# Optimization experiments

Hardware: AMD Instinct MI355X
Metric: run time of the kernel (lower is better)

## Reference

```python
import jax, jax.numpy as jnp
import numpy as np

B, S, N = 8, 64, 256
STATE, IN_F, OUT_F = 128, 64, 64
ALPHA = 0.2
NEG = -9e15


def setup_inputs() -> dict:
    key = jax.random.key(0)
    ks = jax.random.split(key, 12)
    d = {
        "hyper_inputs": jax.random.normal(ks[0], (B, S, STATE), jnp.float32),
        "inputs": jax.random.normal(ks[1], (B, S, N, IN_F), jnp.float32),
        "Adj": jax.random.randint(ks[2], (N, N), 0, 2, jnp.int32),
        # hyper_w: Linear(STATE,32) -> ReLU -> Linear(32, OUT_F*IN_F)
        "w1": jax.random.normal(ks[3], (STATE, 32), jnp.float32) * 0.08,
        "b1": jax.random.normal(ks[4], (32,), jnp.float32) * 0.01,
        "w2": jax.random.normal(ks[5], (32, OUT_F * IN_F), jnp.float32) * 0.08,
        "b2": jax.random.normal(ks[6], (OUT_F * IN_F,), jnp.float32) * 0.01,
        # hyper_a: Linear(STATE,32) -> ReLU -> Linear(32, 2*OUT_F)
        "aw1": jax.random.normal(ks[7], (STATE, 32), jnp.float32) * 0.08,
        "ab1": jax.random.normal(ks[8], (32,), jnp.float32) * 0.01,
        "aw2": jax.random.normal(ks[9], (32, 2 * OUT_F), jnp.float32) * 0.08,
        "ab2": jax.random.normal(ks[10], (2 * OUT_F,), jnp.float32) * 0.01,
    }
    return d


def _leaky(x):
    return jnp.where(x >= 0, x, ALPHA * x)


def reference(hyper_inputs, inputs, Adj, w1, b1, w2, b2, aw1, ab1, aw2, ab2):
    # hypernetwork-generated per-(b,s) weights
    hdn = jax.nn.relu(hyper_inputs @ w1 + b1)            # [B,S,32]
    W = jnp.abs(hdn @ w2 + b2).reshape(B, S, IN_F, OUT_F)
    hda = jax.nn.relu(hyper_inputs @ aw1 + ab1)
    a = jnp.abs(hda @ aw2 + ab2)                          # [B,S,2*OUT_F]

    h = jnp.einsum('bsni,bsio->bsno', inputs, W)          # [B,S,N,OUT_F]

    # decomposed GAT scores: e[b,s,i,j] = leakyrelu(h_i.a1 + h_j.a2)
    a1, a2 = a[..., :OUT_F], a[..., OUT_F:]
    e1 = jnp.einsum('bsno,bso->bsn', h, a1)               # source term
    e2 = jnp.einsum('bsno,bso->bsn', h, a2)               # target term
    e = _leaky(e1[..., :, None] + e2[..., None, :])       # [B,S,N,N]

    attention = jnp.where(Adj > 0, e, NEG)
    # NOTE: faithful to original: softmax over dim=1 (the S axis)
    attention = jax.nn.softmax(attention, axis=1)
    h_prime = jnp.einsum('bsij,bsjo->bsio', attention, h)  # [B,S,N,OUT_F]
    return jax.nn.elu(h_prime)                              # concat=True branch
```

## Files before the change

kernel.cpp:

```cpp
#include <hip/hip_runtime.h>
#include <hip/hip_bf16.h>
#include <math.h>

#define BB 8
#define SS 64
#define NN 256
#define ST 128
#define IF 64
#define OF 64
#define H1 32
#define ALPHA 0.2f

typedef short short8 __attribute__((ext_vector_type(8)));
typedef float f32x4 __attribute__((ext_vector_type(4)));
typedef unsigned short ushort_t;

static __device__ __forceinline__ ushort_t f2bf(float f) {
    __hip_bfloat16 h = __float2bfloat16(f);
    return *reinterpret_cast<ushort_t*>(&h);
}

__global__ __launch_bounds__(512) void k_hyper2(
    const float* __restrict__ hyper,
    const float* __restrict__ w1, const float* __restrict__ b1,
    const float* __restrict__ w2, const float* __restrict__ b2,
    const float* __restrict__ aw1, const float* __restrict__ ab1,
    const float* __restrict__ aw2, const float* __restrict__ ab2,
    float* __restrict__ Wd, float* __restrict__ Aa)
{
    const int t = threadIdx.x;
    const int bs0 = blockIdx.x * 2;
    __shared__ float hy[2][ST];
    __shared__ float hdn_s[2][H1];
    __shared__ float hda_s[2][H1];
    if (t < 2 * ST)
        hy[t >> 7][t & 127] = hyper[(size_t)bs0 * ST + t];
    __syncthreads();
    if (t < 64) {
        const int q = t >> 5, c = t & 31;
        float acc = b1[c];
#pragma unroll 4
        for (int k = 0; k < ST; ++k) acc = fmaf(hy[q][k], w1[k * H1 + c], acc);
        hdn_s[q][c] = fmaxf(acc, 0.f);
    } else if (t < 128) {
        const int tt = t - 64;
        const int q = tt >> 5, c = tt & 31;
        float acc = ab1[c];
#pragma unroll 4
        for (int k = 0; k < ST; ++k) acc = fmaf(hy[q][k], aw1[k * H1 + c], acc);
        hda_s[q][c] = fmaxf(acc, 0.f);
    }
    __syncthreads();
    if (t < 256) {
        const int q = t >> 7, c = t & 127;
        float a = ab2[c];
#pragma unroll
        for (int k = 0; k < H1; ++k)
            a = fmaf(hda_s[q][k], aw2[k * 128 + c], a);
        Aa[(size_t)(bs0 + q) * 128 + c] = fabsf(a);
    }
#pragma unroll
    for (int p = 0; p < 2; ++p) {
        const int e = t * 4 + p * 2048;
        const float4 bb = *(const float4*)&b2[e];
        float4 a0 = bb, a1 = bb;
#pragma unroll
        for (int kq = 0; kq < 8; ++kq) {
            const float4 h0 = *(const float4*)&hdn_s[0][kq * 4];
            const float4 h1 = *(const float4*)&hdn_s[1][kq * 4];
#pragma unroll
            for (int c = 0; c < 4; ++c) {
                const float4 wv = *(const float4*)&w2[(size_t)(kq * 4 + c) * 4096 + e];
                const float s0 = (c == 0) ? h0.x : (c == 1) ? h0.y : (c == 2) ? h0.z : h0.w;
                const float s1 = (c == 0) ? h1.x : (c == 1) ? h1.y : (c == 2) ? h1.z : h1.w;
                a0.x = fmaf(s0, wv.x, a0.x); a0.y = fmaf(s0, wv.y, a0.y);
                a0.z = fmaf(s0, wv.z, a0.z); a0.w = fmaf(s0, wv.w, a0.w);
                a1.x = fmaf(s1, wv.x, a1.x); a1.y = fmaf(s1, wv.y, a1.y);
                a1.z = fmaf(s1, wv.z, a1.z); a1.w = fmaf(s1, wv.w, a1.w);
            }
        }
        a0.x = fabsf(a0.x); a0.y = fabsf(a0.y); a0.z = fabsf(a0.z); a0.w = fabsf(a0.w);
        a1.x = fabsf(a1.x); a1.y = fabsf(a1.y); a1.z = fabsf(a1.z); a1.w = fabsf(a1.w);
        *(float4*)&Wd[(size_t)(bs0 + 0) * 4096 + e] = a0;
        *(float4*)&Wd[(size_t)(bs0 + 1) * 4096 + e] = a1;
    }
}

__global__ __launch_bounds__(256) void k_h(
    const float* __restrict__ x, const float* __restrict__ Wd,
    const float* __restrict__ Aa,
    ushort_t* __restrict__ HbT, float* __restrict__ E1, float* __restrict__ E2)
{
    const int bs = blockIdx.x;
    const int tid = threadIdx.x;
    const int nt = tid >> 3;
    const int ot = tid & 7;
    __shared__ float Wl[IF * OF];
    __shared__ float a1s[OF], a2s[OF];
    {
        const float4* src = (const float4*)(Wd + (size_t)bs * 4096);
        float4* dst = (float4*)Wl;
        for (int p = 0; p < 4; ++p) dst[tid + p * 256] = src[tid + p * 256];
        if (tid < 64) a1s[tid] = Aa[(size_t)bs * 128 + tid];
        else if (tid < 128) a2s[tid - 64] = Aa[(size_t)bs * 128 + tid];
    }
    __syncthreads();

    const float4* xb = (const float4*)(x + ((size_t)bs * NN + nt * 8) * IF);
    float acc[8][8];
#pragma unroll
    for (int r = 0; r < 8; ++r)
#pragma unroll
        for (int c = 0; c < 8; ++c) acc[r][c] = 0.f;

#pragma unroll
    for (int kq = 0; kq < 16; ++kq) {
        float4 xv[8];
#pragma unroll
        for (int r = 0; r < 8; ++r) xv[r] = xb[r * 16 + kq];
#pragma unroll
        for (int c = 0; c < 4; ++c) {
            const int k = kq * 4 + c;
            const float4 w0 = *(const float4*)&Wl[k * OF + ot * 8];
            const float4 w1 = *(const float4*)&Wl[k * OF + ot * 8 + 4];
#pragma unroll
            for (int r = 0; r < 8; ++r) {
                const float xs = (c == 0) ? xv[r].x : (c == 1) ? xv[r].y
                               : (c == 2) ? xv[r].z : xv[r].w;
                acc[r][0] = fmaf(xs, w0.x, acc[r][0]);
                acc[r][1] = fmaf(xs, w0.y, acc[r][1]);
                acc[r][2] = fmaf(xs, w0.z, acc[r][2]);
                acc[r][3] = fmaf(xs, w0.w, acc[r][3]);
                acc[r][4] = fmaf(xs, w1.x, acc[r][4]);
                acc[r][5] = fmaf(xs, w1.y, acc[r][5]);
                acc[r][6] = fmaf(xs, w1.z, acc[r][6]);
                acc[r][7] = fmaf(xs, w1.w, acc[r][7]);
            }
        }
    }

    const float4 av0 = *(const float4*)&a1s[ot * 8];
    const float4 av1 = *(const float4*)&a1s[ot * 8 + 4];
    const float4 bv0 = *(const float4*)&a2s[ot * 8];
    const float4 bv1 = *(const float4*)&a2s[ot * 8 + 4];
    float e1sel = 0.f, e2sel = 0.f;
#pragma unroll
    for (int r = 0; r < 8; ++r) {
        float p1 = acc[r][0]*av0.x + acc[r][1]*av0.y + acc[r][2]*av0.z + acc[r][3]*av0.w
                 + acc[r][4]*av1.x + acc[r][5]*av1.y + acc[r][6]*av1.z + acc[r][7]*av1.w;
        float p2 = acc[r][0]*bv0.x + acc[r][1]*bv0.y + acc[r][2]*bv0.z + acc[r][3]*bv0.w
                 + acc[r][4]*bv1.x + acc[r][5]*bv1.y + acc[r][6]*bv1.z + acc[r][7]*bv1.w;
        p1 += __shfl_xor(p1, 1, 64); p2 += __shfl_xor(p2, 1, 64);
        p1 += __shfl_xor(p1, 2, 64); p2 += __shfl_xor(p2, 2, 64);
        p1 += __shfl_xor(p1, 4, 64); p2 += __shfl_xor(p2, 4, 64);
        if (ot == r) { e1sel = p1; e2sel = p2; }
    }
    E1[(size_t)bs * NN + tid] = e1sel;
    E2[(size_t)bs * NN + tid] = e2sel;

    ushort_t* hb = HbT + (size_t)bs * (OF * NN);
#pragma unroll
    for (int c = 0; c < 8; ++c) {
        short8 pk;
#pragma unroll
        for (int r = 0; r < 8; ++r) pk[r] = (short)f2bf(acc[r][c]);
        *(short8*)(hb + (size_t)(ot * 8 + c) * NN + nt * 8) = pk;
    }
}

__global__ __launch_bounds__(256) void k_softstats(
    const float* __restrict__ E1, const float* __restrict__ E2,
    const int* __restrict__ Adj, unsigned int* __restrict__ MR)
{
    const int bid = blockIdx.x;
    const int b = bid >> 6, i0 = (bid & 63) * 4;
    const int t = threadIdx.x;
    __shared__ float e1s[4][SS];
    {
        const int ii = t >> 6, s = t & 63;
        e1s[ii][s] = E1[(size_t)(b * SS + s) * NN + i0 + ii];
    }
    float e2r[SS];
#pragma unroll
    for (int s = 0; s < SS; ++s)
        e2r[s] = E2[(size_t)(b * SS + s) * NN + t];
    __syncthreads();

#pragma unroll
    for (int ii = 0; ii < 4; ++ii) {
        float mx = -3.0e38f;
#pragma unroll
        for (int s = 0; s < SS; ++s) {
            float v = e1s[ii][s] + e2r[s];
            v = (v >= 0.f) ? v : ALPHA * v;
            mx = fmaxf(mx, v);
        }
        const unsigned int mu = (unsigned int)f2bf(mx);
        const float mUse = __uint_as_float(mu << 16);
        float sum = 0.f;
#pragma unroll
        for (int s = 0; s < SS; ++s) {
            float v = e1s[ii][s] + e2r[s];
            v = (v >= 0.f) ? v : ALPHA * v;
            sum += __expf(v - mUse);
        }
        const int adj = Adj[(size_t)(i0 + ii) * NN + t];
        const float r = (adj > 0) ? (1.f / sum) : -0.015625f;
        MR[(size_t)(b * NN + i0 + ii) * NN + t] =
            (mu << 16) | (unsigned int)f2bf(r);
    }
}

__global__ __launch_bounds__(512) void k_attn(
    const ushort_t* __restrict__ HbT, const float* __restrict__ E1,
    const float* __restrict__ E2, const unsigned int* __restrict__ MR,
    float* __restrict__ out)
{
    const int bs = blockIdx.x;
    const int b = bs >> 6;
    const int tid = threadIdx.x;
    const int wid = tid >> 6;
    const int lane = tid & 63;
    const int l15 = lane & 15;
    const int lhi = lane >> 4;

    __shared__ float e2s[NN];
    if (tid < NN) e2s[tid] = E2[(size_t)bs * NN + tid];
    __syncthreads();

    float e1r[2];
#pragma unroll
    for (int mt = 0; mt < 2; ++mt)
        e1r[mt] = E1[(size_t)bs * NN + wid * 32 + mt * 16 + l15];

    f32x4 acc[2][4];
#pragma unroll
    for (int mt = 0; mt < 2; ++mt)
#pragma unroll
        for (int nt = 0; nt < 4; ++nt) acc[mt][nt] = (f32x4){0.f, 0.f, 0.f, 0.f};

    const ushort_t* hb = HbT + (size_t)bs * (OF * NN);
    const unsigned int* mrb = MR + ((size_t)b * NN) * NN;

    for (int ch = 0; ch < 4; ++ch) {
        short8 bf[4][2];
#pragma unroll
        for (int nt = 0; nt < 4; ++nt) {
            const int o = nt * 16 + l15;
#pragma unroll
            for (int ks = 0; ks < 2; ++ks) {
                const int j0 = ch * 64 + ks * 32 + lhi * 8;
                bf[nt][ks] = *(const short8*)(hb + (size_t)o * NN + j0);
            }
        }
        float e2v[2][8];
#pragma unroll
        for (int ks = 0; ks < 2; ++ks) {
            const int k0 = ch * 64 + ks * 32 + lhi * 8;
            const float4 lo = *(const float4*)&e2s[k0];
            const float4 hi = *(const float4*)&e2s[k0 + 4];
            e2v[ks][0] = lo.x; e2v[ks][1] = lo.y; e2v[ks][2] = lo.z; e2v[ks][3] = lo.w;
            e2v[ks][4] = hi.x; e2v[ks][5] = hi.y; e2v[ks][6] = hi.z; e2v[ks][7] = hi.w;
        }
#pragma unroll
        for (int mt = 0; mt < 2; ++mt) {
            const int row = wid * 32 + mt * 16 + l15;
            const float e1v = e1r[mt];
            const uint4* mrow = (const uint4*)(mrb + (size_t)row * NN);
            short8 af[2];
#pragma unroll
            for (int ks = 0; ks < 2; ++ks) {
                const int k0 = ch * 64 + ks * 32 + lhi * 8;
                const uint4 m0 = mrow[k0 >> 2];
                const uint4 m1 = mrow[(k0 >> 2) + 1];
                const unsigned int wv[8] = {m0.x, m0.y, m0.z, m0.w,
                                            m1.x, m1.y, m1.z, m1.w};
                short8 pk;
#pragma unroll
                for (int kk = 0; kk < 8; ++kk) {
                    const float Mf = __uint_as_float(wv[kk] & 0xFFFF0000u);
                    const float Rf = __uint_as_float(wv[kk] << 16);
                    float v = e1v + e2v[ks][kk];
                    v = (v >= 0.f) ? v : ALPHA * v;
                    const float a = (Rf < 0.f) ? -Rf : __expf(v - Mf) * Rf;
                    pk[kk] = (short)f2bf(a);
                }
                af[ks] = pk;
            }
#pragma unroll
            for (int nt = 0; nt < 4; ++nt) {
                acc[mt][nt] = __builtin_amdgcn_mfma_f32_16x16x32_bf16(
                    af[0], bf[nt][0], acc[mt][nt], 0, 0, 0);
                acc[mt][nt] = __builtin_amdgcn_mfma_f32_16x16x32_bf16(
                    af[1], bf[nt][1], acc[mt][nt], 0, 0, 0);
            }
        }
    }

    float* ob = out + (size_t)bs * (NN * OF);
#pragma unroll
    for (int mt = 0; mt < 2; ++mt) {
        const int rbase = wid * 32 + mt * 16 + lhi * 4;
#pragma unroll
        for (int nt = 0; nt < 4; ++nt) {
            const int o = nt * 16 + l15;
#pragma unroll
            for (int reg = 0; reg < 4; ++reg) {
                float v = acc[mt][nt][reg];
                v = (v > 0.f) ? v : (__expf(v) - 1.f);
                ob[(size_t)(rbase + reg) * OF + o] = v;
            }
        }
    }
}

extern "C" void kernel_launch(void* const* d_in, const int* in_sizes, int n_in,
                              void* d_out, int out_size, void* d_ws, size_t ws_size,
                              hipStream_t stream)
{
    const float* hyper = (const float*)d_in[0];
    const float* x     = (const float*)d_in[1];
    const int*   Adj   = (const int*)d_in[2];
    const float* w1    = (const float*)d_in[3];
    const float* b1    = (const float*)d_in[4];
    const float* w2    = (const float*)d_in[5];
    const float* b2    = (const float*)d_in[6];
    const float* aw1   = (const float*)d_in[7];
    const float* ab1   = (const float*)d_in[8];
    const float* aw2   = (const float*)d_in[9];
    const float* ab2   = (const float*)d_in[10];
    float* out = (float*)d_out;

    float* ws      = (float*)d_ws;
    float* Wd      = ws;
    float* Aa      = Wd + 2097152;
    ushort_t* HbT  = (ushort_t*)(Aa + 65536);
    float* E1      = (float*)(HbT + 8388608);
    float* E2      = E1 + 131072;
    unsigned int* MRp = (unsigned int*)(E2 + 131072);

    k_hyper2<<<dim3(256), dim3(512), 0, stream>>>(hyper, w1, b1, w2, b2,
                                                  aw1, ab1, aw2, ab2, Wd, Aa);
    k_h<<<dim3(512), dim3(256), 0, stream>>>(x, Wd, Aa, HbT, E1, E2);
    k_softstats<<<dim3(512), dim3(256), 0, stream>>>(E1, E2, Adj, MRp);
    k_attn<<<dim3(512), dim3(512), 0, stream>>>(HbT, E1, E2, MRp, out);
}
```

Before: 90.75 us.

## Use bf16 MFMA for projection, fold attention vectors, switch to exp2 math

The per-(b,s) projection h = x·W moves from scalar FP32 FMAs to bf16 MFMA. W is staged transposed in LDS with an XOR swizzle to avoid bank conflicts. E1/E2 are now computed as x·(W·a), pre-scaled by log2(e), so exp2f can replace __expf in the softstats and attention kernels. The softstats kernel caches leaky values in registers instead of recomputing them, and the attention kernel hoists its MR loads ahead of the compute loop. The change trades FP32 precision in h for bf16 inputs to the MFMA.

```diff
diff --git a/kernel.cpp b/kernel.cpp
--- a/kernel.cpp
+++ b/kernel.cpp
@@ -10,8 +10,10 @@
 #define OF 64
 #define H1 32
 #define ALPHA 0.2f
+#define LOG2E 1.4426950408889634f
 
 typedef short short8 __attribute__((ext_vector_type(8)));
+typedef short short4_t __attribute__((ext_vector_type(4)));
 typedef float f32x4 __attribute__((ext_vector_type(4)));
 typedef unsigned short ushort_t;
 
@@ -93,78 +95,122 @@
 {
     const int bs = blockIdx.x;
     const int tid = threadIdx.x;
-    const int nt = tid >> 3;
-    const int ot = tid & 7;
-    __shared__ float Wl[IF * OF];
+    const int wid = tid >> 6;
+    const int lane = tid & 63;
+    const int l15 = lane & 15;
+    const int lhi = lane >> 4;
+
+    __shared__ ushort_t Wt[IF * OF];
+    __shared__ float wa1s[IF], wa2s[IF];
     __shared__ float a1s[OF], a2s[OF];
+
+    if (tid < 64) a1s[tid] = Aa[(size_t)bs * 128 + tid];
+    else if (tid < 128) a2s[tid - 64] = Aa[(size_t)bs * 128 + tid];
+
     {
-        const float4* src = (const float4*)(Wd + (size_t)bs * 4096);
-        float4* dst = (float4*)Wl;
-        for (int p = 0; p < 4; ++p) dst[tid + p * 256] = src[tid + p * 256];
-        if (tid < 64) a1s[tid] = Aa[(size_t)bs * 128 + tid];
-        else if (tid < 128) a2s[tid - 64] = Aa[(size_t)bs * 128 + tid];
-    }
-    __syncthreads();
-
-    const float4* xb = (const float4*)(x + ((size_t)bs * NN + nt * 8) * IF);
-    float acc[8][8];
-#pragma unroll
-    for (int r = 0; r < 8; ++r)
-#pragma unroll
-        for (int c = 0; c < 8; ++c) acc[r][c] = 0.f;
-
-#pragma unroll
-    for (int kq = 0; kq < 16; ++kq) {
-        float4 xv[8];
-#pragma unroll
-        for (int r = 0; r < 8; ++r) xv[r] = xb[r * 16 + kq];
-#pragma unroll
-        for (int c = 0; c < 4; ++c) {
-            const int k = kq * 4 + c;
-            const float4 w0 = *(const float4*)&Wl[k * OF + ot * 8];
-            const float4 w1 = *(const float4*)&Wl[k * OF + ot * 8 + 4];
-#pragma unroll
-            for (int r = 0; r < 8; ++r) {
-                const float xs = (c == 0) ? xv[r].x : (c == 1) ? xv[r].y
-                               : (c == 2) ? xv[r].z : xv[r].w;
-                acc[r][0] = fmaf(xs, w0.x, acc[r][0]);
-                acc[r][1] = fmaf(xs, w0.y, acc[r][1]);
-                acc[r][2] = fmaf(xs, w0.z, acc[r][2]);
-                acc[r][3] = fmaf(xs, w0.w, acc[r][3]);
-                acc[r][4] = fmaf(xs, w1.x, acc[r][4]);
-                acc[r][5] = fmaf(xs, w1.y, acc[r][5]);
-                acc[r][6] = fmaf(xs, w1.z, acc[r][6]);
-                acc[r][7] = fmaf(xs, w1.w, acc[r][7]);
-            }
-        }
-    }
-
-    const float4 av0 = *(const float4*)&a1s[ot * 8];
-    const float4 av1 = *(const float4*)&a1s[ot * 8 + 4];
-    const float4 bv0 = *(const float4*)&a2s[ot * 8];
-    const float4 bv1 = *(const float4*)&a2s[ot * 8 + 4];
-    float e1sel = 0.f, e2sel = 0.f;
-#pragma unroll
-    for (int r = 0; r < 8; ++r) {
-        float p1 = acc[r][0]*av0.x + acc[r][1]*av0.y + acc[r][2]*av0.z + acc[r][3]*av0.w
-                 + acc[r][4]*av1.x + acc[r][5]*av1.y + acc[r][6]*av1.z + acc[r][7]*av1.w;
-        float p2 = acc[r][0]*bv0.x + acc[r][1]*bv0.y + acc[r][2]*bv0.z + acc[r][3]*bv0.w
-                 + acc[r][4]*bv1.x + acc[r][5]*bv1.y + acc[r][6]*bv1.z + acc[r][7]*bv1.w;
-        p1 += __shfl_xor(p1, 1, 64); p2 += __shfl_xor(p2, 1, 64);
-        p1 += __shfl_xor(p1, 2, 64); p2 += __shfl_xor(p2, 2, 64);
-        p1 += __shfl_xor(p1, 4, 64); p2 += __shfl_xor(p2, 4, 64);
-        if (ot == r) { e1sel = p1; e2sel = p2; }
-    }
-    E1[(size_t)bs * NN + tid] = e1sel;
-    E2[(size_t)bs * NN + tid] = e2sel;
+        const float4* w4 = (const float4*)(Wd + (size_t)bs * 4096);
+#pragma unroll
+        for (int p = 0; p < 4; ++p) {
+            const int idx = tid + p * 256;
+            const float4 f = w4[idx];
+            const int k = (idx * 4) >> 6;
+            const int o0 = (idx * 4) & 63;
+            Wt[(o0 + 0) * 64 + (k ^ (((o0 + 0) & 7) << 3))] = f2bf(f.x);
+            Wt[(o0 + 1) * 64 + (k ^ (((o0 + 1) & 7) << 3))] = f2bf(f.y);
+            Wt[(o0 + 2) * 64 + (k ^ (((o0 + 2) & 7) << 3))] = f2bf(f.z);
+            Wt[(o0 + 3) * 64 + (k ^ (((o0 + 3) & 7) << 3))] = f2bf(f.w);
+        }
+    }
+    __syncthreads();
+
+    if (tid < 64) {
+        const float4* wr = (const float4*)(Wd + (size_t)bs * 4096 + tid * 64);
+        float s1 = 0.f, s2 = 0.f;
+#pragma unroll
+        for (int q = 0; q < 16; ++q) {
+            const float4 f = wr[q];
+            const float4 u = *(const float4*)&a1s[q * 4];
+            const float4 v = *(const float4*)&a2s[q * 4];
+            s1 += f.x * u.x + f.y * u.y + f.z * u.z + f.w * u.w;
+            s2 += f.x * v.x + f.y * v.y + f.z * v.z + f.w * v.w;
+        }
+        wa1s[tid] = s1; wa2s[tid] = s2;
+    }
+    __syncthreads();
+
+    {
+        const float4* xr = (const float4*)(x + ((size_t)bs * NN + tid) * IF);
+        float s1 = 0.f, s2 = 0.f;
+#pragma unroll
+        for (int q = 0; q < 16; ++q) {
+            const float4 f = xr[q];
+            const float4 u = *(const float4*)&wa1s[q * 4];
+            const float4 v = *(const float4*)&wa2s[q * 4];
+            s1 += f.x * u.x + f.y * u.y + f.z * u.z + f.w * u.w;
+            s2 += f.x * v.x + f.y * v.y + f.z * v.z + f.w * v.w;
+        }
+        E1[(size_t)bs * NN + tid] = s1 * LOG2E;
+        E2[(size_t)bs * NN + tid] = s2 * LOG2E;
+    }
+
+    f32x4 acc[4][4];
+#pragma unroll
+    for (int mt = 0; mt < 4; ++mt)
+#pragma unroll
+        for (int nt = 0; nt < 4; ++nt) acc[mt][nt] = (f32x4){0.f, 0.f, 0.f, 0.f};
+
+    short8 af[4][2];
+#pragma unroll
+    for (int mt = 0; mt < 4; ++mt) {
+        const int row = wid * 64 + mt * 16 + l15;
+        const float* xrow = x + ((size_t)bs * NN + row) * IF;
+#pragma unroll
+        for (int ks = 0; ks < 2; ++ks) {
+            const int k0 = ks * 32 + lhi * 8;
+            const float4 fa = *(const float4*)&xrow[k0];
+            const float4 fb = *(const float4*)&xrow[k0 + 4];
+            short8 pk;
+            pk[0] = (short)f2bf(fa.x); pk[1] = (short)f2bf(fa.y);
+            pk[2] = (short)f2bf(fa.z); pk[3] = (short)f2bf(fa.w);
+            pk[4] = (short)f2bf(fb.x); pk[5] = (short)f2bf(fb.y);
+            pk[6] = (short)f2bf(fb.z); pk[7] = (short)f2bf(fb.w);
+            af[mt][ks] = pk;
+        }
+    }
+    short8 bfr[4][2];
+#pragma unroll
+    for (int nt = 0; nt < 4; ++nt) {
+        const int o = nt * 16 + l15;
+#pragma unroll
+        for (int ks = 0; ks < 2; ++ks) {
+            const int k0 = ks * 32 + lhi * 8;
+            bfr[nt][ks] = *(const short8*)&Wt[o * 64 + (k0 ^ ((o & 7) << 3))];
+        }
+    }
+#pragma unroll
+    for (int mt = 0; mt < 4; ++mt)
+#pragma unroll
+        for (int nt = 0; nt < 4; ++nt) {
+            acc[mt][nt] = __builtin_amdgcn_mfma_f32_16x16x32_bf16(
+                af[mt][0], bfr[nt][0], acc[mt][nt], 0, 0, 0);
+            acc[mt][nt] = __builtin_amdgcn_mfma_f32_16x16x32_bf16(
+                af[mt][1], bfr[nt][1], acc[mt][nt], 0, 0, 0);
+        }
 
     ushort_t* hb = HbT + (size_t)bs * (OF * NN);
 #pragma unroll
-    for (int c = 0; c < 8; ++c) {
-        short8 pk;
-#pragma unroll
-        for (int r = 0; r < 8; ++r) pk[r] = (short)f2bf(acc[r][c]);
-        *(short8*)(hb + (size_t)(ot * 8 + c) * NN + nt * 8) = pk;
+    for (int mt = 0; mt < 4; ++mt) {
+        const int rbase = wid * 64 + mt * 16 + lhi * 4;
+#pragma unroll
+        for (int nt = 0; nt < 4; ++nt) {
+            const int o = nt * 16 + l15;
+            short4_t pk;
+            pk[0] = (short)f2bf(acc[mt][nt][0]);
+            pk[1] = (short)f2bf(acc[mt][nt][1]);
+            pk[2] = (short)f2bf(acc[mt][nt][2]);
+            pk[3] = (short)f2bf(acc[mt][nt][3]);
+            *(short4_t*)(hb + (size_t)o * NN + rbase) = pk;
+        }
     }
 }
 
@@ -188,22 +234,21 @@
 
 #pragma unroll
     for (int ii = 0; ii < 4; ++ii) {
+        float v[SS];
         float mx = -3.0e38f;
 #pragma unroll
         for (int s = 0; s < SS; ++s) {
-            float v = e1s[ii][s] + e2r[s];
-            v = (v >= 0.f) ? v : ALPHA * v;
-            mx = fmaxf(mx, v);
+            float u = e1s[ii][s] + e2r[s];
+            u = fmaxf(u, ALPHA * u);
+            v[s] = u;
+            mx = fmaxf(mx, u);
         }
         const unsigned int mu = (unsigned int)f2bf(mx);
         const float mUse = __uint_as_float(mu << 16);
         float sum = 0.f;
 #pragma unroll
-        for (int s = 0; s < SS; ++s) {
-            float v = e1s[ii][s] + e2r[s];
-            v = (v >= 0.f) ? v : ALPHA * v;
-            sum += __expf(v - mUse);
-        }
+        for (int s = 0; s < SS; ++s)
+            sum += exp2f(v[s] - mUse);
         const int adj = Adj[(size_t)(i0 + ii) * NN + t];
         const float r = (adj > 0) ? (1.f / sum) : -0.015625f;
         MR[(size_t)(b * NN + i0 + ii) * NN + t] =
@@ -241,17 +286,26 @@
 
     const ushort_t* hb = HbT + (size_t)bs * (OF * NN);
     const unsigned int* mrb = MR + ((size_t)b * NN) * NN;
+    const uint4* mrow0 = (const uint4*)(mrb + (size_t)(wid * 32 + l15) * NN);
+    const uint4* mrow1 = (const uint4*)(mrb + (size_t)(wid * 32 + 16 + l15) * NN);
 
     for (int ch = 0; ch < 4; ++ch) {
-        short8 bf[4][2];
+        short8 bfr[4][2];
 #pragma unroll
         for (int nt = 0; nt < 4; ++nt) {
             const int o = nt * 16 + l15;
 #pragma unroll
             for (int ks = 0; ks < 2; ++ks) {
                 const int j0 = ch * 64 + ks * 32 + lhi * 8;
-                bf[nt][ks] = *(const short8*)(hb + (size_t)o * NN + j0);
-            }
+                bfr[nt][ks] = *(const short8*)(hb + (size_t)o * NN + j0);
+            }
+        }
+        uint4 mq[2][2][2];
+#pragma unroll
+        for (int ks = 0; ks < 2; ++ks) {
+            const int qi = (ch * 64 + ks * 32 + lhi * 8) >> 2;
+            mq[0][ks][0] = mrow0[qi]; mq[0][ks][1] = mrow0[qi + 1];
+            mq[1][ks][0] = mrow1[qi]; mq[1][ks][1] = mrow1[qi + 1];
         }
         float e2v[2][8];
 #pragma unroll
@@ -264,25 +318,21 @@
         }
 #pragma unroll
         for (int mt = 0; mt < 2; ++mt) {
-            const int row = wid * 32 + mt * 16 + l15;
             const float e1v = e1r[mt];
-            const uint4* mrow = (const uint4*)(mrb + (size_t)row * NN);
             short8 af[2];
 #pragma unroll
             for (int ks = 0; ks < 2; ++ks) {
-                const int k0 = ch * 64 + ks * 32 + lhi * 8;
-                const uint4 m0 = mrow[k0 >> 2];
-                const uint4 m1 = mrow[(k0 >> 2) + 1];
-                const unsigned int wv[8] = {m0.x, m0.y, m0.z, m0.w,
-                                            m1.x, m1.y, m1.z, m1.w};
+                const unsigned int wv[8] = {
+                    mq[mt][ks][0].x, mq[mt][ks][0].y, mq[mt][ks][0].z, mq[mt][ks][0].w,
+                    mq[mt][ks][1].x, mq[mt][ks][1].y, mq[mt][ks][1].z, mq[mt][ks][1].w};
                 short8 pk;
 #pragma unroll
                 for (int kk = 0; kk < 8; ++kk) {
                     const float Mf = __uint_as_float(wv[kk] & 0xFFFF0000u);
                     const float Rf = __uint_as_float(wv[kk] << 16);
                     float v = e1v + e2v[ks][kk];
-                    v = (v >= 0.f) ? v : ALPHA * v;
-                    const float a = (Rf < 0.f) ? -Rf : __expf(v - Mf) * Rf;
+                    v = fmaxf(v, ALPHA * v);
+                    const float a = (Rf < 0.f) ? -Rf : exp2f(v - Mf) * Rf;
                     pk[kk] = (short)f2bf(a);
                 }
                 af[ks] = pk;
@@ -290,9 +340,9 @@
 #pragma unroll
             for (int nt = 0; nt < 4; ++nt) {
                 acc[mt][nt] = __builtin_amdgcn_mfma_f32_16x16x32_bf16(
-                    af[0], bf[nt][0], acc[mt][nt], 0, 0, 0);
+                    af[0], bfr[nt][0], acc[mt][nt], 0, 0, 0);
                 acc[mt][nt] = __builtin_amdgcn_mfma_f32_16x16x32_bf16(
-                    af[1], bf[nt][1], acc[mt][nt], 0, 0, 0);
+                    af[1], bfr[nt][1], acc[mt][nt], 0, 0, 0);
             }
         }
     }
```

Measured after the change: 88.20 us. 1.03x faster.
